# Kernel tuning notes

Hardware: AMD Instinct MI355X
Metric: run time of the kernel (lower is better)

The kernel has to match this reference:

```python
import jax, jax.numpy as jnp
import numpy as np


def _cft_icft_matrices(n):
    # Continuous FT over t in [0,1) sampled at n points, frequencies = fftfreq(n, d=1/n).
    # CFT  : X(f) = integral x(t) e^{-2pi i f t} dt  ~=  (1/n) * sum_t x(t) e^{-2pi i f t}
    # ICFT : x(t) = integral X(f) e^{+2pi i f t} df  ~=  df   * sum_f X(f) e^{+2pi i f t}
    # The original module evaluates the ICFT on the fftshift-ed frequency grid while the
    # coefficients stay in fft (unshifted) index order; we reproduce that pairing.
    sr = float(n)
    t = jnp.arange(n, dtype=jnp.float32) / n                      # [n]
    f = jnp.fft.fftfreq(n, d=1.0 / sr).astype(jnp.float32)        # [n], fft order
    f_shift = jnp.fft.fftshift(f)                                 # [n], shifted order
    two_pi = jnp.float32(2.0 * np.pi)
    dt = jnp.float32(1.0 / n)
    df = jnp.float32(sr / n)  # frequency spacing = 1.0 for unit duration
    # E_cft: [n_freq, n_time], E_icft: [n_time, n_freq]
    E_cft = jnp.exp(-1j * two_pi * f[:, None] * t[None, :]).astype(jnp.complex64) * dt
    E_icft = jnp.exp(1j * two_pi * t[:, None] * f_shift[None, :]).astype(jnp.complex64) * df
    return E_cft, E_icft


def setup_inputs() -> dict:
    key = jax.random.key(0)
    k1, k2, k3 = jax.random.split(key, 3)
    B, Ci, Co, n, modes = 32, 64, 64, 4096, 64
    scale = 1.0 / (Ci * Co)
    x = jax.random.normal(k1, (B, Ci, n), dtype=jnp.float32)
    # weights1 = scale * rand(Ci, Co, modes, cfloat): uniform[0,1) real and imag parts
    w_real = scale * jax.random.uniform(k2, (Ci, Co, modes), dtype=jnp.float32)
    w_imag = scale * jax.random.uniform(k3, (Ci, Co, modes), dtype=jnp.float32)
    return {"x": x, "w_real": w_real, "w_imag": w_imag}


def reference(x, w_real, w_imag):
    B, Ci, n = x.shape
    Co, modes = w_real.shape[1], w_real.shape[2]
    E_cft, E_icft = _cft_icft_matrices(n)
    w = (w_real + 1j * w_imag).astype(jnp.complex64)              # [Ci, Co, modes]
    xc = x.astype(jnp.complex64)
    # Batched CFT over all (batch, channel) pairs as one complex GEMM.
    x_cft = jnp.einsum('bit,ft->bif', xc, E_cft)                  # [B, Ci, n]
    # Spectral linear transform on the lowest `modes` frequencies.
    low = jnp.einsum('bif,iof->bof', x_cft[:, :, :modes], w)      # [B, Co, modes]
    out_ft = jnp.zeros((B, Co, n), dtype=jnp.complex64).at[:, :, :modes].set(low)
    # Batched ICFT back to the time grid; module returns the real part.
    out = jnp.einsum('bof,tf->bot', out_ft, E_icft)               # [B, Co, n]
    return out.real
```

## Files before the change

kernel.cpp:

```cpp
#include <hip/hip_runtime.h>
#include <math.h>

#define NT 4096
#define MODES 64
#define ROWS 2048
#define TWO_PI 6.283185307179586f
#define PI_F 3.14159265358979f

static __device__ __forceinline__ void rotm(float& wr, float& wi, float sr, float si) {
  float nr = fmaf(wr, sr, -wi * si);
  float ni = fmaf(wr, si,  wi * sr);
  wr = nr; wi = ni;
}

__global__ __launch_bounds__(256) void cft_fused_kernel(
    const float* __restrict__ x, float2* __restrict__ xfp,
    const float* __restrict__ w_real, const float* __restrict__ w_imag,
    float* __restrict__ wrt, float* __restrict__ wit, int S) {
  __shared__ __align__(16) char smem[25344];
  const int tid = threadIdx.x;
  const int nCft = 64 * S;

  if ((int)blockIdx.x >= nCft) {
    float (*tile)[65] = (float (*)[65])smem;
    const int bx = (int)blockIdx.x - nCft;
    const int sel = bx >> 6;
    const int io0 = (bx & 63) * 64;
    const float* __restrict__ src = sel ? w_imag : w_real;
    float* __restrict__ dst = sel ? wit : wrt;
#pragma unroll
    for (int j = 0; j < 4; ++j) {
      const int idx = tid + j * 256;
      const int r = idx >> 4;
      const int kq = idx & 15;
      float4 v = ((const float4*)src)[(size_t)(io0 + r) * 16 + kq];
      tile[r][4 * kq + 0] = v.x; tile[r][4 * kq + 1] = v.y;
      tile[r][4 * kq + 2] = v.z; tile[r][4 * kq + 3] = v.w;
    }
    __syncthreads();
#pragma unroll
    for (int j = 0; j < 16; ++j) {
      const int idx = tid + j * 256;
      const int k = idx >> 6;
      const int r = idx & 63;
      dst[(size_t)k * 4096 + io0 + r] = tile[r][k];
    }
    return;
  }

  float* xsf = (float*)smem;
  float2* tws = (float2*)(smem + 16896);
  const int k0 = tid & 7;
  const int rg = tid >> 3;
  const int C = 512 / S;
  const int rowblk = (int)blockIdx.x / S;
  const int ts = (int)blockIdx.x % S;
  const int row0 = rowblk * 32;

  const int c4 = k0 & 3;
  const float p  = (c4 & 1) ? -1.f : 1.f;
  const float qc = (c4 == 0) ? 1.f : ((c4 == 2) ? -1.f : 0.f);
  const float rc = (c4 == 1) ? -1.f : ((c4 == 3) ? 1.f : 0.f);
  float Aw, Bw;
  sincosf(-PI_F * (float)k0 * 0.25f, &Bw, &Aw);

  float ar[8] = {0.f,0.f,0.f,0.f,0.f,0.f,0.f,0.f};
  float ai[8] = {0.f,0.f,0.f,0.f,0.f,0.f,0.f,0.f};

  const float4* __restrict__ xg4 = (const float4*)x;
  const float2* bp = (const float2*)(xsf + rg * 132);

  for (int sub = 0; sub < C / 16; ++sub) {
    const int tl0 = ts * C + sub * 16;
    __syncthreads();
#pragma unroll
    for (int it = 0; it < 4; ++it) {
      const int idx = tid + it * 256;
      const int tlf = idx & 3;
      const int j = (idx >> 2) & 7;
      const int row = idx >> 5;
      ((float4*)xsf)[row * 33 + j * 4 + tlf] =
          xg4[(size_t)(row0 + row) * (NT / 4) + j * 128 + (tl0 >> 2) + tlf];
    }
#pragma unroll
    for (int it = 0; it < 4; ++it) {
      const int e = tid + it * 256;
      const int tl = e >> 6;
      const int k = e & 63;
      const int ph = (k * (tl0 + tl)) & (NT - 1);
      float swr, swi;
      sincosf(-TWO_PI * (float)ph / (float)NT, &swi, &swr);
      tws[tl * 66 + k] = make_float2(swr, swi);
    }
    __syncthreads();
#pragma unroll 2
    for (int tt = 0; tt < 8; ++tt) {
      float2 v[8];
#pragma unroll
      for (int j = 0; j < 8; ++j) v[j] = bp[j * 8 + tt];
#pragma unroll
      for (int par = 0; par < 2; ++par) {
        const int tl = 2 * tt + par;
        const float x0 = par ? v[0].y : v[0].x;
        const float x1 = par ? v[1].y : v[1].x;
        const float x2 = par ? v[2].y : v[2].x;
        const float x3 = par ? v[3].y : v[3].x;
        const float x4 = par ? v[4].y : v[4].x;
        const float x5 = par ? v[5].y : v[5].x;
        const float x6 = par ? v[6].y : v[6].x;
        const float x7 = par ? v[7].y : v[7].x;
        const float ue = fmaf(p, x4, x0), ve = fmaf(p, x6, x2);
        const float Er = fmaf(qc, ve, ue), Ei = rc * ve;
        const float uo = fmaf(p, x5, x1), vo = fmaf(p, x7, x3);
        const float Or_ = fmaf(qc, vo, uo), Oi_ = rc * vo;
        float sr = fmaf(Aw, Or_, Er); sr = fmaf(-Bw, Oi_, sr);
        float si = fmaf(Aw, Oi_, Ei); si = fmaf( Bw, Or_, si);
#pragma unroll
        for (int q = 0; q < 8; ++q) {
          const float2 w = tws[tl * 66 + k0 + 8 * q];
          ar[q] = fmaf(sr, w.x, ar[q]); ar[q] = fmaf(-si, w.y, ar[q]);
          ai[q] = fmaf(sr, w.y, ai[q]); ai[q] = fmaf( si, w.x, ai[q]);
        }
      }
    }
  }
  const float dt = 1.0f / (float)NT;
  const size_t base = ((size_t)ts * 64 + rowblk) * 64;
#pragma unroll
  for (int q = 0; q < 8; ++q) {
    xfp[(base + k0 + 8 * q) * 32 + rg] = make_float2(ar[q] * dt, ai[q] * dt);
  }
}

__global__ __launch_bounds__(256) void mix_kernel(
    const float* __restrict__ wrt, const float* __restrict__ wit,
    const float2* __restrict__ xfp, float2* __restrict__ yf_t, int S) {
  __shared__ float2 wsc[4096];
  __shared__ float2 xsh[256];
  const int k = blockIdx.x & 63;
  const int bq = blockIdx.x >> 6;
  const int tid = threadIdx.x;
#pragma unroll
  for (int j = 0; j < 4; ++j) {
    const int idx = tid + 256 * j;
    float4 vr = ((const float4*)(wrt + (size_t)k * 4096))[idx];
    float4 vi = ((const float4*)(wit + (size_t)k * 4096))[idx];
    wsc[4 * idx + 0] = make_float2(vr.x, vi.x);
    wsc[4 * idx + 1] = make_float2(vr.y, vi.y);
    wsc[4 * idx + 2] = make_float2(vr.z, vi.z);
    wsc[4 * idx + 3] = make_float2(vr.w, vi.w);
  }
  {
    const int R = bq * 256 + tid;
    const int rowblk = R >> 5;
    const int rl = R & 31;
    float2 acc = make_float2(0.f, 0.f);
    for (int s = 0; s < S; ++s) {
      float2 v = xfp[(((size_t)s * 64 + rowblk) * 64 + k) * 32 + rl];
      acc.x += v.x; acc.y += v.y;
    }
    xsh[tid] = acc;
  }
  __syncthreads();
  const int o = tid & 63;
  const int bl = tid >> 6;
  float accr = 0.f, acci = 0.f;
#pragma unroll 8
  for (int i = 0; i < 64; ++i) {
    const float2 xv = xsh[bl * 64 + i];
    const float2 w = wsc[i * 64 + o];
    accr = fmaf(xv.x, w.x, accr); accr = fmaf(-xv.y, w.y, accr);
    acci = fmaf(xv.x, w.y, acci); acci = fmaf( xv.y, w.x, acci);
  }
  yf_t[(size_t)k * ROWS + bq * 256 + bl * 64 + o] = make_float2(accr, acci);
}

__global__ __launch_bounds__(256) void icft_kernel(const float2* __restrict__ yf_t,
                                                   float* __restrict__ out) {
  __shared__ float2 ysh[4][66];
  const int rgrp = blockIdx.x >> 1;
  const int tc = blockIdx.x & 1;
  const int row0 = rgrp * 4;
  const int tid = threadIdx.x;
  {
    const int k = tid >> 2;
    const int r = tid & 3;
    ysh[r][k] = yf_t[(size_t)k * ROWS + row0 + r];
  }
  __syncthreads();
  const int tl = tc * 256 + tid;
  float stepr, stepi;
  sincosf(TWO_PI * (float)tl / (float)NT, &stepi, &stepr);
  float wr = 1.f, wi = 0.f;
  float Gr[8][4] = {{0.f}};
  float Gi[8][4] = {{0.f}};
  for (int m = 0; m < 8; ++m) {
#pragma unroll
    for (int cc = 0; cc < 8; ++cc) {
      const int k = 8 * m + cc;
#pragma unroll
      for (int r = 0; r < 4; ++r) {
        const float2 y = ysh[r][k];
        Gr[cc][r] = fmaf(y.x, wr, Gr[cc][r]);
        Gr[cc][r] = fmaf(-y.y, wi, Gr[cc][r]);
        if (cc != 0 && cc != 4) {
          Gi[cc][r] = fmaf(y.x, wi, Gi[cc][r]);
          Gi[cc][r] = fmaf(y.y, wr, Gi[cc][r]);
        }
      }
      rotm(wr, wi, stepr, stepi);
    }
  }
  const float KK = 0.7071067811865476f;
  const float sgn = (tl & 1) ? -1.f : 1.f;
#pragma unroll
  for (int r = 0; r < 4; ++r) {
    const float Ae = (Gr[0][r] + Gr[2][r]) + (Gr[4][r] + Gr[6][r]);
    const float Ao = (Gr[1][r] + Gr[3][r]) + (Gr[5][r] + Gr[7][r]);
    const float A2 = (Gr[0][r] - Gr[2][r]) + (Gr[4][r] - Gr[6][r]);
    const float B2 = (Gi[1][r] - Gi[3][r]) + (Gi[5][r] - Gi[7][r]);
    const float P  = Gr[0][r] - Gr[4][r];
    const float Qr = (Gr[1][r] - Gr[3][r]) - (Gr[5][r] - Gr[7][r]);
    const float R  = Gi[6][r] - Gi[2][r];
    const float Qi = (Gi[5][r] - Gi[1][r]) + (Gi[7][r] - Gi[3][r]);
    const float U = P + R, V = P - R;
    const float W1 = KK * (Qr + Qi), W2 = KK * (Qr - Qi);
    float* op = out + (size_t)(row0 + r) * NT + tl;
    op[0]    = sgn * (Ae + Ao);
    op[512]  = sgn * (U + W1);
    op[1024] = sgn * (A2 - B2);
    op[1536] = sgn * (V - W2);
    op[2048] = sgn * (Ae - Ao);
    op[2560] = sgn * (U - W1);
    op[3072] = sgn * (A2 + B2);
    op[3584] = sgn * (V + W2);
  }
}

extern "C" void kernel_launch(void* const* d_in, const int* in_sizes, int n_in,
                              void* d_out, int out_size, void* d_ws, size_t ws_size,
                              hipStream_t stream) {
  const float* x      = (const float*)d_in[0];
  const float* w_real = (const float*)d_in[1];
  const float* w_imag = (const float*)d_in[2];
  float* out = (float*)d_out;

  const size_t MB = (size_t)ROWS * MODES * sizeof(float2);
  int S = 16;
  while (S > 4 && (size_t)(S + 4) * MB > ws_size) S >>= 1;

  char* wsp = (char*)d_ws;
  float2* xfp  = (float2*)wsp;
  float2* yf_t = (float2*)(wsp + (size_t)S * MB);
  float*  wrt  = (float*)(wsp + (size_t)(S + 2) * MB);
  float*  wit  = (float*)(wsp + (size_t)(S + 3) * MB);

  cft_fused_kernel<<<64 * S + 128, 256, 0, stream>>>(x, xfp, w_real, w_imag,
                                                     wrt, wit, S);
  mix_kernel<<<512, 256, 0, stream>>>(wrt, wit, xfp, yf_t, S);
  icft_kernel<<<1024, 256, 0, stream>>>(yf_t, out);
}
```

Before: 47.63 us.

## Replace shared-memory twiddle tables with register recurrences and readlane broadcasts

```diff
diff --git a/kernel.cpp b/kernel.cpp
--- a/kernel.cpp
+++ b/kernel.cpp
@@ -17,7 +17,7 @@
     const float* __restrict__ x, float2* __restrict__ xfp,
     const float* __restrict__ w_real, const float* __restrict__ w_imag,
     float* __restrict__ wrt, float* __restrict__ wit, int S) {
-  __shared__ __align__(16) char smem[25344];
+  __shared__ __align__(16) char smem[16896];
   const int tid = threadIdx.x;
   const int nCft = 64 * S;
 
@@ -49,13 +49,13 @@
   }
 
   float* xsf = (float*)smem;
-  float2* tws = (float2*)(smem + 16896);
   const int k0 = tid & 7;
   const int rg = tid >> 3;
   const int C = 512 / S;
   const int rowblk = (int)blockIdx.x / S;
   const int ts = (int)blockIdx.x % S;
   const int row0 = rowblk * 32;
+  const int tl0b = ts * C;
 
   const int c4 = k0 & 3;
   const float p  = (c4 & 1) ? -1.f : 1.f;
@@ -64,6 +64,30 @@
   float Aw, Bw;
   sincosf(-PI_F * (float)k0 * 0.25f, &Bw, &Aw);
 
+  float wAr[8], wAi[8], wBr[8], wBi[8], s2r[8], s2i[8];
+  {
+    float bAr, bAi, m8r, m8i, b1r, b1i, b2r, b2i;
+    sincosf(-TWO_PI * (float)((k0 * tl0b) & (NT - 1)) / (float)NT, &bAi, &bAr);
+    sincosf(-TWO_PI * (float)((8 * tl0b) & (NT - 1)) / (float)NT, &m8i, &m8r);
+    sincosf(-TWO_PI * (float)k0 / (float)NT, &b1i, &b1r);
+    sincosf(-TWO_PI * (float)(2 * k0) / (float)NT, &b2i, &b2r);
+    const float c8r = 0.9999247018391445f,  c8i = -0.0122715382857199f;
+    const float c16r = 0.9996988186962042f, c16i = -0.0245412285229123f;
+    float aR = bAr, aI = bAi;
+    float s1R = b1r, s1I = b1i;
+    float t2R = b2r, t2I = b2i;
+#pragma unroll
+    for (int q = 0; q < 8; ++q) {
+      wAr[q] = aR; wAi[q] = aI;
+      wBr[q] = fmaf(aR, s1R, -aI * s1I);
+      wBi[q] = fmaf(aR, s1I,  aI * s1R);
+      s2r[q] = t2R; s2i[q] = t2I;
+      rotm(aR, aI, m8r, m8i);
+      rotm(s1R, s1I, c8r, c8i);
+      rotm(t2R, t2I, c16r, c16i);
+    }
+  }
+
   float ar[8] = {0.f,0.f,0.f,0.f,0.f,0.f,0.f,0.f};
   float ai[8] = {0.f,0.f,0.f,0.f,0.f,0.f,0.f,0.f};
 
@@ -71,7 +95,7 @@
   const float2* bp = (const float2*)(xsf + rg * 132);
 
   for (int sub = 0; sub < C / 16; ++sub) {
-    const int tl0 = ts * C + sub * 16;
+    const int tl0 = tl0b + sub * 16;
     __syncthreads();
 #pragma unroll
     for (int it = 0; it < 4; ++it) {
@@ -82,16 +106,6 @@
       ((float4*)xsf)[row * 33 + j * 4 + tlf] =
           xg4[(size_t)(row0 + row) * (NT / 4) + j * 128 + (tl0 >> 2) + tlf];
     }
-#pragma unroll
-    for (int it = 0; it < 4; ++it) {
-      const int e = tid + it * 256;
-      const int tl = e >> 6;
-      const int k = e & 63;
-      const int ph = (k * (tl0 + tl)) & (NT - 1);
-      float swr, swi;
-      sincosf(-TWO_PI * (float)ph / (float)NT, &swi, &swr);
-      tws[tl * 66 + k] = make_float2(swr, swi);
-    }
     __syncthreads();
 #pragma unroll 2
     for (int tt = 0; tt < 8; ++tt) {
@@ -100,7 +114,6 @@
       for (int j = 0; j < 8; ++j) v[j] = bp[j * 8 + tt];
 #pragma unroll
       for (int par = 0; par < 2; ++par) {
-        const int tl = 2 * tt + par;
         const float x0 = par ? v[0].y : v[0].x;
         const float x1 = par ? v[1].y : v[1].x;
         const float x2 = par ? v[2].y : v[2].x;
@@ -117,10 +130,16 @@
         float si = fmaf(Aw, Oi_, Ei); si = fmaf( Bw, Or_, si);
 #pragma unroll
         for (int q = 0; q < 8; ++q) {
-          const float2 w = tws[tl * 66 + k0 + 8 * q];
-          ar[q] = fmaf(sr, w.x, ar[q]); ar[q] = fmaf(-si, w.y, ar[q]);
-          ai[q] = fmaf(sr, w.y, ai[q]); ai[q] = fmaf( si, w.x, ai[q]);
+          const float wr = par ? wBr[q] : wAr[q];
+          const float wi = par ? wBi[q] : wAi[q];
+          ar[q] = fmaf(sr, wr, ar[q]); ar[q] = fmaf(-si, wi, ar[q]);
+          ai[q] = fmaf(sr, wi, ai[q]); ai[q] = fmaf( si, wr, ai[q]);
         }
+      }
+#pragma unroll
+      for (int q = 0; q < 8; ++q) {
+        rotm(wAr[q], wAi[q], s2r[q], s2i[q]);
+        rotm(wBr[q], wBi[q], s2r[q], s2i[q]);
       }
     }
   }
@@ -173,6 +192,10 @@
     acci = fmaf(xv.x, w.y, acci); acci = fmaf( xv.y, w.x, acci);
   }
   yf_t[(size_t)k * ROWS + bq * 256 + bl * 64 + o] = make_float2(accr, acci);
+}
+
+static __device__ __forceinline__ float rlane(float v, int k) {
+  return __int_as_float(__builtin_amdgcn_readlane(__float_as_int(v), k));
 }
 
 __global__ __launch_bounds__(256) void icft_kernel(const float2* __restrict__ yf_t,
@@ -188,6 +211,13 @@
     ysh[r][k] = yf_t[(size_t)k * ROWS + row0 + r];
   }
   __syncthreads();
+  const int lane = tid & 63;
+  float yLr[4], yLi[4];
+#pragma unroll
+  for (int r = 0; r < 4; ++r) {
+    const float2 y = ysh[r][lane];
+    yLr[r] = y.x; yLi[r] = y.y;
+  }
   const int tl = tc * 256 + tid;
   float stepr, stepi;
   sincosf(TWO_PI * (float)tl / (float)NT, &stepi, &stepr);
@@ -200,12 +230,13 @@
       const int k = 8 * m + cc;
 #pragma unroll
       for (int r = 0; r < 4; ++r) {
-        const float2 y = ysh[r][k];
-        Gr[cc][r] = fmaf(y.x, wr, Gr[cc][r]);
-        Gr[cc][r] = fmaf(-y.y, wi, Gr[cc][r]);
+        const float yx = rlane(yLr[r], k);
+        const float yy = rlane(yLi[r], k);
+        Gr[cc][r] = fmaf(yx, wr, Gr[cc][r]);
+        Gr[cc][r] = fmaf(-yy, wi, Gr[cc][r]);
         if (cc != 0 && cc != 4) {
-          Gi[cc][r] = fmaf(y.x, wi, Gi[cc][r]);
-          Gi[cc][r] = fmaf(y.y, wr, Gi[cc][r]);
+          Gi[cc][r] = fmaf(yx, wi, Gi[cc][r]);
+          Gi[cc][r] = fmaf(yy, wr, Gi[cc][r]);
         }
       }
       rotm(wr, wi, stepr, stepi);
```

After: 52.94 us. 11.1% more time.

## Compute CFT with bf16 MFMA using split-precision input and precomputed twiddle matrix

Applied to the files above, without the earlier changes.

```diff
diff --git a/kernel.cpp b/kernel.cpp
--- a/kernel.cpp
+++ b/kernel.cpp
@@ -5,7 +5,9 @@
 #define MODES 64
 #define ROWS 2048
 #define TWO_PI 6.283185307179586f
-#define PI_F 3.14159265358979f
+
+typedef __attribute__((ext_vector_type(8))) short bf16x8;
+typedef __attribute__((ext_vector_type(4))) float f32x4;
 
 static __device__ __forceinline__ void rotm(float& wr, float& wi, float sr, float si) {
   float nr = fmaf(wr, sr, -wi * si);
@@ -13,11 +15,35 @@
   wr = nr; wi = ni;
 }
 
-__global__ __launch_bounds__(256) void cft_fused_kernel(
-    const float* __restrict__ x, float2* __restrict__ xfp,
+static __device__ __forceinline__ unsigned short bf16rn(float x) {
+  unsigned u = __float_as_uint(x);
+  u += 0x7FFFu + ((u >> 16) & 1u);
+  return (unsigned short)(u >> 16);
+}
+
+__global__ __launch_bounds__(256) void bgen_kernel(unsigned short* __restrict__ Bg) {
+  const int e0 = ((int)blockIdx.x * 256 + (int)threadIdx.x) * 8;
+  const int n = e0 >> 12;
+  const int t0 = e0 & 4095;
+  const int k = (n < 64) ? n : (n - 64);
+  bf16x8 pack;
+#pragma unroll
+  for (int j = 0; j < 8; ++j) {
+    const int ph = (k * (t0 + j)) & (NT - 1);
+    float s, c;
+    sincosf(TWO_PI * (float)ph / (float)NT, &s, &c);
+    const float v = ((n < 64) ? c : -s) * (1.0f / (float)NT);
+    pack[j] = (short)bf16rn(v);
+  }
+  *(bf16x8*)(Bg + e0) = pack;
+}
+
+__global__ __launch_bounds__(256) void cft_mfma_kernel(
+    const float* __restrict__ x, const unsigned short* __restrict__ Bg,
+    float* __restrict__ xfp,
     const float* __restrict__ w_real, const float* __restrict__ w_imag,
     float* __restrict__ wrt, float* __restrict__ wit, int S) {
-  __shared__ __align__(16) char smem[25344];
+  __shared__ __align__(16) char smem[24576];
   const int tid = threadIdx.x;
   const int nCft = 64 * S;
 
@@ -48,93 +74,100 @@
     return;
   }
 
-  float* xsf = (float*)smem;
-  float2* tws = (float2*)(smem + 16896);
-  const int k0 = tid & 7;
-  const int rg = tid >> 3;
-  const int C = 512 / S;
+  unsigned short* Ah = (unsigned short*)smem;
+  unsigned short* Al = (unsigned short*)(smem + 4096);
+  unsigned short* Bs = (unsigned short*)(smem + 8192);
+
   const int rowblk = (int)blockIdx.x / S;
   const int ts = (int)blockIdx.x % S;
   const int row0 = rowblk * 32;
-
-  const int c4 = k0 & 3;
-  const float p  = (c4 & 1) ? -1.f : 1.f;
-  const float qc = (c4 == 0) ? 1.f : ((c4 == 2) ? -1.f : 0.f);
-  const float rc = (c4 == 1) ? -1.f : ((c4 == 3) ? 1.f : 0.f);
-  float Aw, Bw;
-  sincosf(-PI_F * (float)k0 * 0.25f, &Bw, &Aw);
-
-  float ar[8] = {0.f,0.f,0.f,0.f,0.f,0.f,0.f,0.f};
-  float ai[8] = {0.f,0.f,0.f,0.f,0.f,0.f,0.f,0.f};
-
-  const float4* __restrict__ xg4 = (const float4*)x;
-  const float2* bp = (const float2*)(xsf + rg * 132);
-
-  for (int sub = 0; sub < C / 16; ++sub) {
-    const int tl0 = ts * C + sub * 16;
+  const int t0 = ts * (NT / S);
+  const int subs = (NT / S) / 64;
+
+  const int lane = tid & 63;
+  const int w = tid >> 6;
+
+  f32x4 acc[2][2];
+#pragma unroll
+  for (int mt = 0; mt < 2; ++mt)
+#pragma unroll
+    for (int nt = 0; nt < 2; ++nt) acc[mt][nt] = (f32x4){0.f, 0.f, 0.f, 0.f};
+
+  const int aru = tid & 7;
+  const int arow = tid >> 3;
+
+  for (int sub = 0; sub < subs; ++sub) {
+    const int tb = t0 + sub * 64;
     __syncthreads();
+    {
+      const float* xp = x + (size_t)(row0 + arow) * NT + tb + aru * 8;
+      const float4 v0 = *(const float4*)xp;
+      const float4 v1 = *(const float4*)(xp + 4);
+      float xv[8] = {v0.x, v0.y, v0.z, v0.w, v1.x, v1.y, v1.z, v1.w};
+      bf16x8 ph, pl;
+#pragma unroll
+      for (int j = 0; j < 8; ++j) {
+        const unsigned short h = bf16rn(xv[j]);
+        ph[j] = (short)h;
+        const float hf = __uint_as_float((unsigned)h << 16);
+        pl[j] = (short)bf16rn(xv[j] - hf);
+      }
+      const int col = (aru ^ (arow & 7)) * 8;
+      *(bf16x8*)(Ah + arow * 64 + col) = ph;
+      *(bf16x8*)(Al + arow * 64 + col) = pl;
+    }
 #pragma unroll
     for (int it = 0; it < 4; ++it) {
       const int idx = tid + it * 256;
-      const int tlf = idx & 3;
-      const int j = (idx >> 2) & 7;
-      const int row = idx >> 5;
-      ((float4*)xsf)[row * 33 + j * 4 + tlf] =
-          xg4[(size_t)(row0 + row) * (NT / 4) + j * 128 + (tl0 >> 2) + tlf];
-    }
-#pragma unroll
-    for (int it = 0; it < 4; ++it) {
-      const int e = tid + it * 256;
-      const int tl = e >> 6;
-      const int k = e & 63;
-      const int ph = (k * (tl0 + tl)) & (NT - 1);
-      float swr, swi;
-      sincosf(-TWO_PI * (float)ph / (float)NT, &swi, &swr);
-      tws[tl * 66 + k] = make_float2(swr, swi);
+      const int ku = idx & 7;
+      const int n = idx >> 3;
+      const bf16x8 v = *(const bf16x8*)(Bg + (size_t)n * NT + tb + ku * 8);
+      const int col = (ku ^ (n & 7)) * 8;
+      *(bf16x8*)(Bs + n * 64 + col) = v;
     }
     __syncthreads();
-#pragma unroll 2
-    for (int tt = 0; tt < 8; ++tt) {
-      float2 v[8];
-#pragma unroll
-      for (int j = 0; j < 8; ++j) v[j] = bp[j * 8 + tt];
-#pragma unroll
-      for (int par = 0; par < 2; ++par) {
-        const int tl = 2 * tt + par;
-        const float x0 = par ? v[0].y : v[0].x;
-        const float x1 = par ? v[1].y : v[1].x;
-        const float x2 = par ? v[2].y : v[2].x;
-        const float x3 = par ? v[3].y : v[3].x;
-        const float x4 = par ? v[4].y : v[4].x;
-        const float x5 = par ? v[5].y : v[5].x;
-        const float x6 = par ? v[6].y : v[6].x;
-        const float x7 = par ? v[7].y : v[7].x;
-        const float ue = fmaf(p, x4, x0), ve = fmaf(p, x6, x2);
-        const float Er = fmaf(qc, ve, ue), Ei = rc * ve;
-        const float uo = fmaf(p, x5, x1), vo = fmaf(p, x7, x3);
-        const float Or_ = fmaf(qc, vo, uo), Oi_ = rc * vo;
-        float sr = fmaf(Aw, Or_, Er); sr = fmaf(-Bw, Oi_, sr);
-        float si = fmaf(Aw, Oi_, Ei); si = fmaf( Bw, Or_, si);
-#pragma unroll
-        for (int q = 0; q < 8; ++q) {
-          const float2 w = tws[tl * 66 + k0 + 8 * q];
-          ar[q] = fmaf(sr, w.x, ar[q]); ar[q] = fmaf(-si, w.y, ar[q]);
-          ai[q] = fmaf(sr, w.y, ai[q]); ai[q] = fmaf( si, w.x, ai[q]);
+    const int kg = lane >> 4;
+#pragma unroll
+    for (int ks = 0; ks < 2; ++ks) {
+      bf16x8 bf[2];
+#pragma unroll
+      for (int nt = 0; nt < 2; ++nt) {
+        const int n = w * 32 + nt * 16 + (lane & 15);
+        const int col = ((ks * 4 + kg) ^ (n & 7)) * 8;
+        bf[nt] = *(const bf16x8*)(Bs + n * 64 + col);
+      }
+#pragma unroll
+      for (int mt = 0; mt < 2; ++mt) {
+        const int row = mt * 16 + (lane & 15);
+        const int col = ((ks * 4 + kg) ^ (row & 7)) * 8;
+        const bf16x8 ah = *(const bf16x8*)(Ah + row * 64 + col);
+        const bf16x8 al = *(const bf16x8*)(Al + row * 64 + col);
+#pragma unroll
+        for (int nt = 0; nt < 2; ++nt) {
+          acc[mt][nt] = __builtin_amdgcn_mfma_f32_16x16x32_bf16(ah, bf[nt], acc[mt][nt], 0, 0, 0);
+          acc[mt][nt] = __builtin_amdgcn_mfma_f32_16x16x32_bf16(al, bf[nt], acc[mt][nt], 0, 0, 0);
         }
       }
     }
   }
-  const float dt = 1.0f / (float)NT;
-  const size_t base = ((size_t)ts * 64 + rowblk) * 64;
-#pragma unroll
-  for (int q = 0; q < 8; ++q) {
-    xfp[(base + k0 + 8 * q) * 32 + rg] = make_float2(ar[q] * dt, ai[q] * dt);
+  const int nb = w * 32 + (lane & 15);
+#pragma unroll
+  for (int nt = 0; nt < 2; ++nt) {
+    const int n = nb + nt * 16;
+    const int plane = n >> 6;
+    const int kk = n & 63;
+#pragma unroll
+    for (int mt = 0; mt < 2; ++mt) {
+      const int rl = mt * 16 + (lane >> 4) * 4;
+      float4 st = {acc[mt][nt][0], acc[mt][nt][1], acc[mt][nt][2], acc[mt][nt][3]};
+      ((float4*)xfp)[((((size_t)ts * 64 + rowblk) * 2 + plane) * 64 + kk) * 8 + (rl >> 2)] = st;
+    }
   }
 }
 
 __global__ __launch_bounds__(256) void mix_kernel(
     const float* __restrict__ wrt, const float* __restrict__ wit,
-    const float2* __restrict__ xfp, float2* __restrict__ yf_t, int S) {
+    const float* __restrict__ xfp, float2* __restrict__ yf_t, int S) {
   __shared__ float2 wsc[4096];
   __shared__ float2 xsh[256];
   const int k = blockIdx.x & 63;
@@ -156,8 +189,9 @@
     const int rl = R & 31;
     float2 acc = make_float2(0.f, 0.f);
     for (int s = 0; s < S; ++s) {
-      float2 v = xfp[(((size_t)s * 64 + rowblk) * 64 + k) * 32 + rl];
-      acc.x += v.x; acc.y += v.y;
+      const size_t b0 = (((size_t)s * 64 + rowblk) * 2) * 2048;
+      acc.x += xfp[b0 + (size_t)k * 32 + rl];
+      acc.y += xfp[b0 + 2048 + (size_t)k * 32 + rl];
     }
     xsh[tid] = acc;
   }
@@ -247,16 +281,18 @@
 
   const size_t MB = (size_t)ROWS * MODES * sizeof(float2);
   int S = 16;
-  while (S > 4 && (size_t)(S + 4) * MB > ws_size) S >>= 1;
+  while (S > 4 && (size_t)(S + 5) * MB > ws_size) S >>= 1;
 
   char* wsp = (char*)d_ws;
-  float2* xfp  = (float2*)wsp;
+  float*  xfp  = (float*)wsp;
   float2* yf_t = (float2*)(wsp + (size_t)S * MB);
   float*  wrt  = (float*)(wsp + (size_t)(S + 2) * MB);
   float*  wit  = (float*)(wsp + (size_t)(S + 3) * MB);
-
-  cft_fused_kernel<<<64 * S + 128, 256, 0, stream>>>(x, xfp, w_real, w_imag,
-                                                     wrt, wit, S);
+  unsigned short* Bg = (unsigned short*)(wsp + (size_t)(S + 4) * MB);
+
+  bgen_kernel<<<256, 256, 0, stream>>>(Bg);
+  cft_mfma_kernel<<<64 * S + 128, 256, 0, stream>>>(x, Bg, xfp, w_real, w_imag,
+                                                    wrt, wit, S);
   mix_kernel<<<512, 256, 0, stream>>>(wrt, wit, xfp, yf_t, S);
   icft_kernel<<<1024, 256, 0, stream>>>(yf_t, out);
 }
```

New measurement: 46.00 us. -3.4%, faster.
